# Performance work log

Measured on AMD Instinct MI355X. Metric: run time of the kernel, lower is better.

Reference implementation:

```python
import jax, jax.numpy as jnp
import numpy as np

G = 8          # n_games
D_IN = 512     # per-game input dim (equal for all games)
H1 = 1024
H2 = 1024
A = 128        # max_actions
B = 8192       # batch rows


def setup_inputs() -> dict:
    key = jax.random.key(0)
    ks = jax.random.split(key, 9)
    state = jax.random.normal(ks[0], (B, D_IN), dtype=jnp.float32)
    idx = jax.random.randint(ks[1], (B,), 0, G, dtype=jnp.int32)
    # per-game input linears: uniform(-1/sqrt(fan_in), 1/sqrt(fan_in))
    lim1 = 1.0 / np.sqrt(D_IN)
    W1 = jax.random.uniform(ks[2], (G, D_IN, H1), minval=-lim1, maxval=lim1, dtype=jnp.float32)
    b1 = jax.random.uniform(ks[3], (G, H1), minval=-lim1, maxval=lim1, dtype=jnp.float32)
    # shared linear
    lim2 = 1.0 / np.sqrt(H1)
    W2 = jax.random.uniform(ks[4], (H1, H2), minval=-lim2, maxval=lim2, dtype=jnp.float32)
    b2 = jax.random.uniform(ks[5], (H2,), minval=-lim2, maxval=lim2, dtype=jnp.float32)
    # per-game output heads: uniform(-0.003, 0.003)
    W3 = jax.random.uniform(ks[6], (G, H2, A), minval=-0.003, maxval=0.003, dtype=jnp.float32)
    b3 = jax.random.uniform(ks[7], (G, A), minval=-0.003, maxval=0.003, dtype=jnp.float32)
    return {"state": state, "idx": idx, "W1": W1, "b1": b1, "W2": W2, "b2": b2, "W3": W3, "b3": b3}


def reference(state, idx, W1, b1, W2, b2, W3, b3):
    # Torch code concatenates per-game groups in sorted-unique-idx order,
    # i.e. a stable permutation of rows by idx; reproduce exactly.
    perm = jnp.argsort(idx, stable=True)          # [B]
    s = state[perm]                               # [B, D_IN]
    g = idx[perm]                                 # [B] game of each permuted row
    # routed first layer: compute all games then gather per-row game
    h1_all = jnp.einsum('bd,gdh->bgh', s, W1) + b1            # [B, G, H1]
    h1 = jax.nn.relu(jnp.take_along_axis(h1_all, g[:, None, None], axis=1)[:, 0, :])  # [B, H1]
    h_f = jax.nn.relu(h1 @ W2 + b2)                            # [B, H2]
    a = jnp.tanh(jnp.einsum('bh,gha->bga', h_f, W3) + b3)      # [B, G, A]
    # NOTE: original gathers heads with the ORIGINAL (unpermuted) idx,
    # even though rows of `a` are in permuted order. Reproduce faithfully.
    out = jnp.take_along_axis(a, idx[:, None, None], axis=1)[:, 0, :]  # [B, A]
    return out
```

## Files before the change

kernel.cpp:

```cpp
#include <hip/hip_runtime.h>
#include <math.h>

#define G_GAMES 8
#define D_IN 512
#define H1 1024
#define H2 1024
#define A_DIM 128
#define B_ROWS 8192

typedef short bf16x8 __attribute__((ext_vector_type(8)));
typedef float f32x4 __attribute__((ext_vector_type(4)));

#define WS_OFF   0u
#define WS_PERM  256u
#define WS_SPERM 33280u
#define WS_W1T   (WS_SPERM + B_ROWS*D_IN*2u)
#define WS_W2T   (WS_W1T + G_GAMES*D_IN*H1*2u)
#define WS_W3T   (WS_W2T + (unsigned)H1*H2*2u)
#define WS_H1    (WS_W3T + G_GAMES*H2*A_DIM*2u)
#define WS_HF    WS_SPERM

__device__ __forceinline__ unsigned short f2bf(float x) {
  union { float f; unsigned int u; } v; v.f = x;
  unsigned int r = v.u + 0x7fffu + ((v.u >> 16) & 1u);
  return (unsigned short)(r >> 16);
}

__device__ __forceinline__ void async_load16(const void* gptr, void* ldsptr) {
  __builtin_amdgcn_global_load_lds(
      (const __attribute__((address_space(1))) unsigned int*)gptr,
      (__attribute__((address_space(3))) unsigned int*)ldsptr,
      16, 0, 0);
}

__device__ void sort_256(const int* __restrict__ idx, int* __restrict__ perm,
                         int* __restrict__ off) {
  __shared__ int wtot[4][9];
  __shared__ int wbase[4][9];
  __shared__ int offs[9];
  const int t = threadIdx.x, lane = t & 63, wave = t >> 6;
  int my[32];
#pragma unroll
  for (int i = 0; i < 8; ++i) {
    const int4 a = *(const int4*)(idx + t * 32 + i * 4);
    my[i*4+0] = a.x; my[i*4+1] = a.y; my[i*4+2] = a.z; my[i*4+3] = a.w;
  }
  int local[8] = {0,0,0,0,0,0,0,0};
#pragma unroll
  for (int i = 0; i < 32; ++i) local[my[i]]++;
  int incl[8];
#pragma unroll
  for (int g = 0; g < 8; ++g) {
    int v = local[g];
#pragma unroll
    for (int d = 1; d < 64; d <<= 1) {
      const int n = __shfl_up(v, d);
      if (lane >= d) v += n;
    }
    incl[g] = v;
  }
  if (lane == 63) {
#pragma unroll
    for (int g = 0; g < 8; ++g) wtot[wave][g] = incl[g];
  }
  __syncthreads();
  if (t < 8) {
    int s = 0;
#pragma unroll
    for (int w = 0; w < 4; ++w) { wbase[w][t] = s; s += wtot[w][t]; }
    wtot[0][t] = s;
  }
  __syncthreads();
  if (t == 0) {
    int s = 0;
#pragma unroll
    for (int g = 0; g < 8; ++g) { offs[g] = s; off[g] = s; s += wtot[0][g]; }
    offs[8] = s; off[8] = s;
  }
  __syncthreads();
  int start[8];
#pragma unroll
  for (int g = 0; g < 8; ++g)
    start[g] = offs[g] + wbase[wave][g] + (incl[g] - local[g]);
#pragma unroll
  for (int i = 0; i < 32; ++i) {
    const int g = my[i];
    perm[start[g]++] = t * 32 + i;
  }
}

__device__ void trans_tile(const float* __restrict__ in,
                           unsigned short* __restrict__ out,
                           int R, int C, int xt, int yt, int z) {
  in  += (size_t)z * R * C;
  out += (size_t)z * R * C;
  __shared__ float tile[64][65];
  const int c0 = xt * 64, r0 = yt * 64;
  const int tx = threadIdx.x & 63, ty = threadIdx.x >> 6;
#pragma unroll
  for (int rr = ty; rr < 64; rr += 4)
    tile[rr][tx] = in[(size_t)(r0 + rr) * C + c0 + tx];
  __syncthreads();
#pragma unroll
  for (int cc = ty; cc < 64; cc += 4)
    out[(size_t)(c0 + cc) * R + r0 + tx] = f2bf(tile[tx][cc]);
}

__global__ __launch_bounds__(256) void k_pre1(const float* __restrict__ W1,
                                              const float* __restrict__ W2,
                                              const float* __restrict__ W3,
                                              const int* __restrict__ idx,
                                              unsigned short* __restrict__ W1T,
                                              unsigned short* __restrict__ W2T,
                                              unsigned short* __restrict__ W3T,
                                              int* __restrict__ perm,
                                              int* __restrict__ off) {
  const int b = blockIdx.x;
  if (b < 1024) {
    const int z = b >> 7, r = b & 127;
    trans_tile(W1, W1T, D_IN, H1, r & 15, r >> 4, z);
  } else if (b < 1280) {
    const int r = b - 1024;
    trans_tile(W2, W2T, H1, H2, r & 15, r >> 4, 0);
  } else if (b < 1536) {
    const int r = (b - 1280) & 31, z = (b - 1280) >> 5;
    trans_tile(W3, W3T, H2, A_DIM, r & 1, r >> 1, z);
  } else {
    sort_256(idx, perm, off);
  }
}

__global__ __launch_bounds__(256) void k_gather(const float* __restrict__ state,
                                                const int* __restrict__ perm,
                                                unsigned short* __restrict__ sPerm) {
  const int p = blockIdx.x * 2 + (threadIdx.x >> 7);
  const int c = (threadIdx.x & 127) << 2;
  const int src = perm[p];
  const float4 v = *(const float4*)(state + (size_t)src * D_IN + c);
  ushort4 o;
  o.x = f2bf(v.x); o.y = f2bf(v.y); o.z = f2bf(v.z); o.w = f2bf(v.w);
  *(ushort4*)(sPerm + (size_t)p * D_IN + c) = o;
}

template <int KTOT>
__device__ __forceinline__ void gemm_db_core(const unsigned short* const* aP,
                                             const unsigned short* const* bP,
                                             char* smem, int tid, f32x4 acc[4][4]) {
  const int lane = tid & 63, wave = tid >> 6;
  const int wm = wave & 1, wn = wave >> 1;
  const int sw = lane & 15, quad = lane >> 4;
  const int mA = wm * 64 + sw;
  const int nB = wn * 64 + sw;
  char* A0 = smem;          char* A1 = smem + 16384;
  char* B0 = smem + 32768;  char* B1 = smem + 49152;
  const int NIT = KTOT >> 6;
#pragma unroll
  for (int c = 0; c < 4; ++c) {
    async_load16(aP[c], A0 + (wave * 32 + c * 8) * 128);
    async_load16(bP[c], B0 + (wave * 32 + c * 8) * 128);
  }
#pragma unroll 2
  for (int k = 0; k < NIT; ++k) {
    __syncthreads();
    char* A = (k & 1) ? A1 : A0;
    char* B = (k & 1) ? B1 : B0;
    if (k + 1 < NIT) {
      char* An = (k & 1) ? A0 : A1;
      char* Bn = (k & 1) ? B0 : B1;
      const int koff = (k + 1) << 6;
#pragma unroll
      for (int c = 0; c < 4; ++c) {
        async_load16(aP[c] + koff, An + (wave * 32 + c * 8) * 128);
        async_load16(bP[c] + koff, Bn + (wave * 32 + c * 8) * 128);
      }
    }
#pragma unroll
    for (int ks = 0; ks < 2; ++ks) {
      const int u = ((((ks << 2) + quad) ^ (sw & 7)) << 4);
      bf16x8 aF[4], bF[4];
#pragma unroll
      for (int i = 0; i < 4; ++i) {
        aF[i] = *(const bf16x8*)(A + (mA + i * 16) * 128 + u);
        bF[i] = *(const bf16x8*)(B + (nB + i * 16) * 128 + u);
      }
#pragma unroll
      for (int i = 0; i < 4; ++i)
#pragma unroll
        for (int j = 0; j < 4; ++j)
          acc[i][j] = __builtin_amdgcn_mfma_f32_16x16x32_bf16(aF[i], bF[j], acc[i][j], 0, 0, 0);
    }
  }
}

__device__ __forceinline__ bool seg_map(const int* __restrict__ off, int T,
                                        int& g, int& seg1, int& row0) {
  int base = 0;
  for (int gg = 0; gg < 8; ++gg) {
    const int s = off[gg], e = off[gg + 1];
    const int nt = (e - s + 127) >> 7;
    if (T < base + nt) { g = gg; seg1 = e; row0 = s + (T - base) * 128; return true; }
    base += nt;
  }
  return false;
}

__device__ __forceinline__ bool seg_map32(const int* __restrict__ off, int T,
                                          int& g, int& seg1, int& row0) {
  int base = 0;
  for (int gg = 0; gg < 8; ++gg) {
    const int s = off[gg], e = off[gg + 1];
    const int nt = (e - s + 31) >> 5;
    if (T < base + nt) { g = gg; seg1 = e; row0 = s + (T - base) * 32; return true; }
    base += nt;
  }
  return false;
}

__device__ __forceinline__ void epilogue_bf16(char* smem, const f32x4 acc[4][4],
                                              const float* bj, int tid,
                                              unsigned short* __restrict__ outp,
                                              size_t ldOut, int row0, int col0,
                                              int vrows) {
  const int lane = tid & 63, wave = tid >> 6;
  const int wm = wave & 1, wn = wave >> 1;
  const int sw = lane & 15, quad = lane >> 4;
  __syncthreads();
#pragma unroll
  for (int i = 0; i < 4; ++i)
#pragma unroll
    for (int j = 0; j < 4; ++j)
#pragma unroll
      for (int r = 0; r < 4; ++r) {
        const int row = wm * 64 + i * 16 + quad * 4 + r;
        const int col = wn * 64 + j * 16 + sw;
        const float v = fmaxf(acc[i][j][r] + bj[j], 0.0f);
        *(unsigned short*)(smem + row * 264 + col * 2) = f2bf(v);
      }
  __syncthreads();
#pragma unroll
  for (int q = 0; q < 8; ++q) {
    const int idxq = q * 256 + tid;
    const int row = idxq >> 4, ch = idxq & 15;
    if (row < vrows) {
      const uint2 lo = *(const uint2*)(smem + row * 264 + ch * 16);
      const uint2 hi = *(const uint2*)(smem + row * 264 + ch * 16 + 8);
      uint4 v; v.x = lo.x; v.y = lo.y; v.z = hi.x; v.w = hi.y;
      *(uint4*)((char*)outp + ((size_t)(row0 + row) * ldOut + col0 + ch * 8) * 2) = v;
    }
  }
}

__global__ __launch_bounds__(256) void k_gemm1(const unsigned short* __restrict__ sPerm,
                                               const unsigned short* __restrict__ W1T,
                                               const float* __restrict__ b1,
                                               const int* __restrict__ off,
                                               unsigned short* __restrict__ h1out) {
  __shared__ char smem[65536];
  int g, seg1, row0;
  if (!seg_map(off, blockIdx.x, g, seg1, row0)) return;
  const int col0 = blockIdx.y * 128;
  const int tid = threadIdx.x, lane = tid & 63, wave = tid >> 6;
  const int gcol = ((lane & 7) ^ (lane >> 3)) << 3;
  const unsigned short* aP[4];
  const unsigned short* bP[4];
#pragma unroll
  for (int c = 0; c < 4; ++c) {
    const int rl = wave * 32 + c * 8 + (lane >> 3);
    int p = row0 + rl;
    if (p > seg1 - 1) p = seg1 - 1;
    aP[c] = sPerm + (size_t)p * D_IN + gcol;
    bP[c] = W1T + (size_t)g * H1 * D_IN + (size_t)(col0 + rl) * D_IN + gcol;
  }
  f32x4 acc[4][4] = {};
  gemm_db_core<D_IN>(aP, bP, smem, tid, acc);
  const int wn = wave >> 1, sw = lane & 15;
  const float* bg = b1 + g * H1;
  float bj[4];
#pragma unroll
  for (int j = 0; j < 4; ++j) bj[j] = bg[col0 + wn * 64 + j * 16 + sw];
  const int vrows = min(128, seg1 - row0);
  epilogue_bf16(smem, acc, bj, tid, h1out, H1, row0, col0, vrows);
}

__global__ __launch_bounds__(256) void k_gemm2(const unsigned short* __restrict__ h1in,
                                               const unsigned short* __restrict__ W2T,
                                               const float* __restrict__ b2,
                                               unsigned short* __restrict__ hfout) {
  __shared__ char smem[65536];
  const int row0 = blockIdx.x * 128, col0 = blockIdx.y * 128;
  const int tid = threadIdx.x, lane = tid & 63, wave = tid >> 6;
  const int gcol = ((lane & 7) ^ (lane >> 3)) << 3;
  const unsigned short* aP[4];
  const unsigned short* bP[4];
#pragma unroll
  for (int c = 0; c < 4; ++c) {
    const int rl = wave * 32 + c * 8 + (lane >> 3);
    aP[c] = h1in + (size_t)(row0 + rl) * H1 + gcol;
    bP[c] = W2T + (size_t)(col0 + rl) * H1 + gcol;
  }
  f32x4 acc[4][4] = {};
  gemm_db_core<H1>(aP, bP, smem, tid, acc);
  const int wn = wave >> 1, sw = lane & 15;
  float bj[4];
#pragma unroll
  for (int j = 0; j < 4; ++j) bj[j] = b2[col0 + wn * 64 + j * 16 + sw];
  epilogue_bf16(smem, acc, bj, tid, hfout, H2, row0, col0, 128);
}

__global__ __launch_bounds__(256) void k_gemm3(const unsigned short* __restrict__ hf,
                                               const unsigned short* __restrict__ W3T,
                                               const float* __restrict__ b3,
                                               const int* __restrict__ off,
                                               const int* __restrict__ perm,
                                               float* __restrict__ outp) {
  __shared__ char smem[40960];
  int g, seg1, row0;
  if (!seg_map32(off, blockIdx.x, g, seg1, row0)) return;
  const int tid = threadIdx.x, lane = tid & 63, wave = tid >> 6;
  const int wm = wave & 1, wn = wave >> 1;
  const int sw = lane & 15, quad = lane >> 4;
  const int gcol = ((lane & 7) ^ (lane >> 3)) << 3;
  int q0 = row0 + wave * 8 + (lane >> 3);
  if (q0 > seg1 - 1) q0 = seg1 - 1;
  const unsigned short* aP = hf + (size_t)perm[q0] * H2 + gcol;
  const unsigned short* bP[4];
#pragma unroll
  for (int c = 0; c < 4; ++c) {
    const int rl = wave * 32 + c * 8 + (lane >> 3);
    bP[c] = W3T + (size_t)g * A_DIM * H2 + (size_t)rl * H2 + gcol;
  }
  char* A0 = smem;         char* A1 = smem + 4096;
  char* B0 = smem + 8192;  char* B1 = smem + 24576;
  const int mA = wm * 16 + sw;
  const int nB = wn * 64 + sw;
  f32x4 acc[4] = {};
  async_load16(aP, A0 + (wave * 8) * 128);
#pragma unroll
  for (int c = 0; c < 4; ++c)
    async_load16(bP[c], B0 + (wave * 32 + c * 8) * 128);
#pragma unroll 2
  for (int k = 0; k < (H2 >> 6); ++k) {
    __syncthreads();
    char* A = (k & 1) ? A1 : A0;
    char* B = (k & 1) ? B1 : B0;
    if (k + 1 < (H2 >> 6)) {
      char* An = (k & 1) ? A0 : A1;
      char* Bn = (k & 1) ? B0 : B1;
      const int koff = (k + 1) << 6;
      async_load16(aP + koff, An + (wave * 8) * 128);
#pragma unroll
      for (int c = 0; c < 4; ++c)
        async_load16(bP[c] + koff, Bn + (wave * 32 + c * 8) * 128);
    }
#pragma unroll
    for (int ks = 0; ks < 2; ++ks) {
      const int u = ((((ks << 2) + quad) ^ (sw & 7)) << 4);
      const bf16x8 aF = *(const bf16x8*)(A + mA * 128 + u);
      bf16x8 bF[4];
#pragma unroll
      for (int j = 0; j < 4; ++j)
        bF[j] = *(const bf16x8*)(B + (nB + j * 16) * 128 + u);
#pragma unroll
      for (int j = 0; j < 4; ++j)
        acc[j] = __builtin_amdgcn_mfma_f32_16x16x32_bf16(aF, bF[j], acc[j], 0, 0, 0);
    }
  }
  const float* bg = b3 + g * A_DIM;
  float bj[4];
#pragma unroll
  for (int j = 0; j < 4; ++j) bj[j] = bg[wn * 64 + j * 16 + sw];
  __syncthreads();
#pragma unroll
  for (int j = 0; j < 4; ++j)
#pragma unroll
    for (int r = 0; r < 4; ++r) {
      const int row = wm * 16 + quad * 4 + r;
      const int col = wn * 64 + j * 16 + sw;
      *(float*)(smem + row * 528 + col * 4) = tanhf(acc[j][r] + bj[j]);
    }
  __syncthreads();
#pragma unroll
  for (int qq = 0; qq < 4; ++qq) {
    const int idxq = qq * 256 + tid;
    const int row = idxq >> 5, ch = idxq & 31;
    if (row0 + row < seg1) {
      const uint4 v = *(const uint4*)(smem + row * 528 + ch * 16);
      *(uint4*)((char*)outp + ((size_t)perm[row0 + row] * A_DIM + ch * 4) * 4) = v;
    }
  }
}

extern "C" void kernel_launch(void* const* d_in, const int* in_sizes, int n_in,
                              void* d_out, int out_size, void* d_ws, size_t ws_size,
                              hipStream_t stream) {
  (void)in_sizes; (void)n_in; (void)out_size; (void)ws_size;
  const float* state = (const float*)d_in[0];
  const int*   idx   = (const int*)d_in[1];
  const float* W1    = (const float*)d_in[2];
  const float* b1    = (const float*)d_in[3];
  const float* W2    = (const float*)d_in[4];
  const float* b2    = (const float*)d_in[5];
  const float* W3    = (const float*)d_in[6];
  const float* b3    = (const float*)d_in[7];
  float* outp = (float*)d_out;
  char* ws = (char*)d_ws;
  int* off  = (int*)(ws + WS_OFF);
  int* perm = (int*)(ws + WS_PERM);
  unsigned short* sPerm = (unsigned short*)(ws + WS_SPERM);
  unsigned short* W1T   = (unsigned short*)(ws + WS_W1T);
  unsigned short* W2T   = (unsigned short*)(ws + WS_W2T);
  unsigned short* W3T   = (unsigned short*)(ws + WS_W3T);
  unsigned short* h1    = (unsigned short*)(ws + WS_H1);
  unsigned short* hf    = (unsigned short*)(ws + WS_HF);

  hipLaunchKernelGGL(k_pre1, dim3(1537), dim3(256), 0, stream,
                     W1, W2, W3, idx, W1T, W2T, W3T, perm, off);
  hipLaunchKernelGGL(k_gather, dim3(B_ROWS / 2), dim3(256), 0, stream, state, perm, sPerm);
  hipLaunchKernelGGL(k_gemm1, dim3(72, 8), dim3(256), 0, stream, sPerm, W1T, b1, off, h1);
  hipLaunchKernelGGL(k_gemm2, dim3(64, 8), dim3(256), 0, stream, h1, W2T, b2, hf);
  hipLaunchKernelGGL(k_gemm3, dim3(264), dim3(256), 0, stream, hf, W3T, b3, off, perm, outp);
}
```

Measured before the change: 155.6 us.

## Load weight B fragments directly from global memory instead of staging in LDS

All three GEMM kernels stop staging the weight (B) tiles through shared memory. Each wave now reads its bf16x8 MFMA fragments straight from global memory inside the k-loop, and only the activation (A) tiles stay double-buffered in LDS. This cuts LDS use per block (64KB to about 33KB), which may allow more blocks per CU, and removes the LDS write and read for B. The cost is that the global B loads are no longer prefetched, so their latency sits exposed right before the MFMAs. Each fragment read is also a strided 16-byte access, and the two waves sharing the same N columns now fetch them redundantly.

```diff
diff --git a/kernel.cpp b/kernel.cpp
--- a/kernel.cpp
+++ b/kernel.cpp
@@ -143,46 +143,41 @@
 }
 
 template <int KTOT>
-__device__ __forceinline__ void gemm_db_core(const unsigned short* const* aP,
-                                             const unsigned short* const* bP,
+__device__ __forceinline__ void gemm_bd_core(const unsigned short* const* aP,
+                                             const unsigned short* __restrict__ bBase,
                                              char* smem, int tid, f32x4 acc[4][4]) {
   const int lane = tid & 63, wave = tid >> 6;
-  const int wm = wave & 1, wn = wave >> 1;
+  const int wm = wave & 1;
   const int sw = lane & 15, quad = lane >> 4;
   const int mA = wm * 64 + sw;
-  const int nB = wn * 64 + sw;
-  char* A0 = smem;          char* A1 = smem + 16384;
-  char* B0 = smem + 32768;  char* B1 = smem + 49152;
+  char* A0 = smem;
+  char* A1 = smem + 16384;
   const int NIT = KTOT >> 6;
 #pragma unroll
-  for (int c = 0; c < 4; ++c) {
+  for (int c = 0; c < 4; ++c)
     async_load16(aP[c], A0 + (wave * 32 + c * 8) * 128);
-    async_load16(bP[c], B0 + (wave * 32 + c * 8) * 128);
-  }
 #pragma unroll 2
   for (int k = 0; k < NIT; ++k) {
     __syncthreads();
     char* A = (k & 1) ? A1 : A0;
-    char* B = (k & 1) ? B1 : B0;
     if (k + 1 < NIT) {
       char* An = (k & 1) ? A0 : A1;
-      char* Bn = (k & 1) ? B0 : B1;
       const int koff = (k + 1) << 6;
 #pragma unroll
-      for (int c = 0; c < 4; ++c) {
+      for (int c = 0; c < 4; ++c)
         async_load16(aP[c] + koff, An + (wave * 32 + c * 8) * 128);
-        async_load16(bP[c] + koff, Bn + (wave * 32 + c * 8) * 128);
-      }
     }
 #pragma unroll
     for (int ks = 0; ks < 2; ++ks) {
       const int u = ((((ks << 2) + quad) ^ (sw & 7)) << 4);
+      const int kg = (k << 6) + (ks << 5);
       bf16x8 aF[4], bF[4];
 #pragma unroll
-      for (int i = 0; i < 4; ++i) {
+      for (int j = 0; j < 4; ++j)
+        bF[j] = *(const bf16x8*)(bBase + (size_t)j * 16 * KTOT + kg);
+#pragma unroll
+      for (int i = 0; i < 4; ++i)
         aF[i] = *(const bf16x8*)(A + (mA + i * 16) * 128 + u);
-        bF[i] = *(const bf16x8*)(B + (nB + i * 16) * 128 + u);
-      }
 #pragma unroll
       for (int i = 0; i < 4; ++i)
 #pragma unroll
@@ -255,25 +250,26 @@
                                                const float* __restrict__ b1,
                                                const int* __restrict__ off,
                                                unsigned short* __restrict__ h1out) {
-  __shared__ char smem[65536];
+  __shared__ char smem[33792];
   int g, seg1, row0;
   if (!seg_map(off, blockIdx.x, g, seg1, row0)) return;
   const int col0 = blockIdx.y * 128;
   const int tid = threadIdx.x, lane = tid & 63, wave = tid >> 6;
+  const int sw = lane & 15, quad = lane >> 4;
   const int gcol = ((lane & 7) ^ (lane >> 3)) << 3;
   const unsigned short* aP[4];
-  const unsigned short* bP[4];
 #pragma unroll
   for (int c = 0; c < 4; ++c) {
     const int rl = wave * 32 + c * 8 + (lane >> 3);
     int p = row0 + rl;
     if (p > seg1 - 1) p = seg1 - 1;
     aP[c] = sPerm + (size_t)p * D_IN + gcol;
-    bP[c] = W1T + (size_t)g * H1 * D_IN + (size_t)(col0 + rl) * D_IN + gcol;
-  }
+  }
+  const unsigned short* bBase =
+      W1T + (size_t)g * H1 * D_IN + (size_t)(col0 + (wave >> 1) * 64 + sw) * D_IN + quad * 8;
   f32x4 acc[4][4] = {};
-  gemm_db_core<D_IN>(aP, bP, smem, tid, acc);
-  const int wn = wave >> 1, sw = lane & 15;
+  gemm_bd_core<D_IN>(aP, bBase, smem, tid, acc);
+  const int wn = wave >> 1;
   const float* bg = b1 + g * H1;
   float bj[4];
 #pragma unroll
@@ -286,21 +282,22 @@
                                                const unsigned short* __restrict__ W2T,
                                                const float* __restrict__ b2,
                                                unsigned short* __restrict__ hfout) {
-  __shared__ char smem[65536];
+  __shared__ char smem[33792];
   const int row0 = blockIdx.x * 128, col0 = blockIdx.y * 128;
   const int tid = threadIdx.x, lane = tid & 63, wave = tid >> 6;
+  const int sw = lane & 15, quad = lane >> 4;
   const int gcol = ((lane & 7) ^ (lane >> 3)) << 3;
   const unsigned short* aP[4];
-  const unsigned short* bP[4];
 #pragma unroll
   for (int c = 0; c < 4; ++c) {
     const int rl = wave * 32 + c * 8 + (lane >> 3);
     aP[c] = h1in + (size_t)(row0 + rl) * H1 + gcol;
-    bP[c] = W2T + (size_t)(col0 + rl) * H1 + gcol;
-  }
+  }
+  const unsigned short* bBase =
+      W2T + (size_t)(col0 + (wave >> 1) * 64 + sw) * H1 + quad * 8;
   f32x4 acc[4][4] = {};
-  gemm_db_core<H1>(aP, bP, smem, tid, acc);
-  const int wn = wave >> 1, sw = lane & 15;
+  gemm_bd_core<H1>(aP, bBase, smem, tid, acc);
+  const int wn = wave >> 1;
   float bj[4];
 #pragma unroll
   for (int j = 0; j < 4; ++j) bj[j] = b2[col0 + wn * 64 + j * 16 + sw];
@@ -313,7 +310,7 @@
                                                const int* __restrict__ off,
                                                const int* __restrict__ perm,
                                                float* __restrict__ outp) {
-  __shared__ char smem[40960];
+  __shared__ char smem[16896];
   int g, seg1, row0;
   if (!seg_map32(off, blockIdx.x, g, seg1, row0)) return;
   const int tid = threadIdx.x, lane = tid & 63, wave = tid >> 6;
@@ -323,43 +320,30 @@
   int q0 = row0 + wave * 8 + (lane >> 3);
   if (q0 > seg1 - 1) q0 = seg1 - 1;
   const unsigned short* aP = hf + (size_t)perm[q0] * H2 + gcol;
-  const unsigned short* bP[4];
-#pragma unroll
-  for (int c = 0; c < 4; ++c) {
-    const int rl = wave * 32 + c * 8 + (lane >> 3);
-    bP[c] = W3T + (size_t)g * A_DIM * H2 + (size_t)rl * H2 + gcol;
-  }
-  char* A0 = smem;         char* A1 = smem + 4096;
-  char* B0 = smem + 8192;  char* B1 = smem + 24576;
+  const unsigned short* bBase =
+      W3T + (size_t)g * A_DIM * H2 + (size_t)(wn * 64 + sw) * H2 + quad * 8;
+  char* A0 = smem;
+  char* A1 = smem + 4096;
   const int mA = wm * 16 + sw;
-  const int nB = wn * 64 + sw;
   f32x4 acc[4] = {};
   async_load16(aP, A0 + (wave * 8) * 128);
-#pragma unroll
-  for (int c = 0; c < 4; ++c)
-    async_load16(bP[c], B0 + (wave * 32 + c * 8) * 128);
 #pragma unroll 2
   for (int k = 0; k < (H2 >> 6); ++k) {
     __syncthreads();
     char* A = (k & 1) ? A1 : A0;
-    char* B = (k & 1) ? B1 : B0;
     if (k + 1 < (H2 >> 6)) {
       char* An = (k & 1) ? A0 : A1;
-      char* Bn = (k & 1) ? B0 : B1;
-      const int koff = (k + 1) << 6;
-      async_load16(aP + koff, An + (wave * 8) * 128);
-#pragma unroll
-      for (int c = 0; c < 4; ++c)
-        async_load16(bP[c] + koff, Bn + (wave * 32 + c * 8) * 128);
+      async_load16(aP + ((k + 1) << 6), An + (wave * 8) * 128);
     }
 #pragma unroll
     for (int ks = 0; ks < 2; ++ks) {
       const int u = ((((ks << 2) + quad) ^ (sw & 7)) << 4);
+      const int kg = (k << 6) + (ks << 5);
       const bf16x8 aF = *(const bf16x8*)(A + mA * 128 + u);
       bf16x8 bF[4];
 #pragma unroll
       for (int j = 0; j < 4; ++j)
-        bF[j] = *(const bf16x8*)(B + (nB + j * 16) * 128 + u);
+        bF[j] = *(const bf16x8*)(bBase + (size_t)j * 16 * H2 + kg);
 #pragma unroll
       for (int j = 0; j < 4; ++j)
         acc[j] = __builtin_amdgcn_mfma_f32_16x16x32_bf16(aF, bF[j], acc[j], 0, 0, 0);
```

New measurement: 209.4 us. 1.35x slower.

## Fuse row gather and bf16 conversion into gemm1 A-tile loads; XCD-aware gemm2 grid

Applied to the files above, without the earlier changes.

Removes the separate gather kernel. gemm1 now reads permuted fp32 state rows directly through perm, converts them to bf16 in registers and writes them into swizzled LDS while the previous tile computes. This drops one launch and the sPerm round trip through global memory. In exchange, A loads now go through registers as synchronous global loads, and each 128-row tile is re-read by all 8 column blocks. gemm2 also switches to a 1D grid remapped so blocks on the same XCD share the same row tiles, aiming for better L2 reuse.

```diff
diff --git a/kernel.cpp b/kernel.cpp
--- a/kernel.cpp
+++ b/kernel.cpp
@@ -130,16 +130,157 @@
   }
 }
 
-__global__ __launch_bounds__(256) void k_gather(const float* __restrict__ state,
-                                                const int* __restrict__ perm,
-                                                unsigned short* __restrict__ sPerm) {
-  const int p = blockIdx.x * 2 + (threadIdx.x >> 7);
-  const int c = (threadIdx.x & 127) << 2;
-  const int src = perm[p];
-  const float4 v = *(const float4*)(state + (size_t)src * D_IN + c);
-  ushort4 o;
-  o.x = f2bf(v.x); o.y = f2bf(v.y); o.z = f2bf(v.z); o.w = f2bf(v.w);
-  *(ushort4*)(sPerm + (size_t)p * D_IN + c) = o;
+__device__ __forceinline__ bool seg_map(const int* __restrict__ off, int T,
+                                        int& g, int& seg1, int& row0) {
+  int base = 0;
+  for (int gg = 0; gg < 8; ++gg) {
+    const int s = off[gg], e = off[gg + 1];
+    const int nt = (e - s + 127) >> 7;
+    if (T < base + nt) { g = gg; seg1 = e; row0 = s + (T - base) * 128; return true; }
+    base += nt;
+  }
+  return false;
+}
+
+__device__ __forceinline__ bool seg_map32(const int* __restrict__ off, int T,
+                                          int& g, int& seg1, int& row0) {
+  int base = 0;
+  for (int gg = 0; gg < 8; ++gg) {
+    const int s = off[gg], e = off[gg + 1];
+    const int nt = (e - s + 31) >> 5;
+    if (T < base + nt) { g = gg; seg1 = e; row0 = s + (T - base) * 32; return true; }
+    base += nt;
+  }
+  return false;
+}
+
+__device__ __forceinline__ void epilogue_bf16(char* smem, const f32x4 acc[4][4],
+                                              const float* bj, int tid,
+                                              unsigned short* __restrict__ outp,
+                                              size_t ldOut, int row0, int col0,
+                                              int vrows) {
+  const int lane = tid & 63, wave = tid >> 6;
+  const int wm = wave & 1, wn = wave >> 1;
+  const int sw = lane & 15, quad = lane >> 4;
+  __syncthreads();
+#pragma unroll
+  for (int i = 0; i < 4; ++i)
+#pragma unroll
+    for (int j = 0; j < 4; ++j)
+#pragma unroll
+      for (int r = 0; r < 4; ++r) {
+        const int row = wm * 64 + i * 16 + quad * 4 + r;
+        const int col = wn * 64 + j * 16 + sw;
+        const float v = fmaxf(acc[i][j][r] + bj[j], 0.0f);
+        *(unsigned short*)(smem + row * 264 + col * 2) = f2bf(v);
+      }
+  __syncthreads();
+#pragma unroll
+  for (int q = 0; q < 8; ++q) {
+    const int idxq = q * 256 + tid;
+    const int row = idxq >> 4, ch = idxq & 15;
+    if (row < vrows) {
+      const uint2 lo = *(const uint2*)(smem + row * 264 + ch * 16);
+      const uint2 hi = *(const uint2*)(smem + row * 264 + ch * 16 + 8);
+      uint4 v; v.x = lo.x; v.y = lo.y; v.z = hi.x; v.w = hi.y;
+      *(uint4*)((char*)outp + ((size_t)(row0 + row) * ldOut + col0 + ch * 8) * 2) = v;
+    }
+  }
+}
+
+__device__ __forceinline__ void write_a_row(char* Ab, const float4* pv, int r, int h) {
+#pragma unroll
+  for (int j = 0; j < 4; ++j) {
+    const float4 a = pv[2 * j], b = pv[2 * j + 1];
+    uint4 w;
+    w.x = (unsigned)f2bf(a.x) | ((unsigned)f2bf(a.y) << 16);
+    w.y = (unsigned)f2bf(a.z) | ((unsigned)f2bf(a.w) << 16);
+    w.z = (unsigned)f2bf(b.x) | ((unsigned)f2bf(b.y) << 16);
+    w.w = (unsigned)f2bf(b.z) | ((unsigned)f2bf(b.w) << 16);
+    *(uint4*)(Ab + r * 128 + (((h * 4 + j) ^ (r & 7)) << 4)) = w;
+  }
+}
+
+__global__ __launch_bounds__(256) void k_gemm1(const float* __restrict__ state,
+                                               const int* __restrict__ perm,
+                                               const unsigned short* __restrict__ W1T,
+                                               const float* __restrict__ b1,
+                                               const int* __restrict__ off,
+                                               unsigned short* __restrict__ h1out) {
+  __shared__ char smem[65536];
+  int g, seg1, row0;
+  if (!seg_map(off, blockIdx.x, g, seg1, row0)) return;
+  const int col0 = blockIdx.y * 128;
+  const int tid = threadIdx.x, lane = tid & 63, wave = tid >> 6;
+  const int gcol = ((lane & 7) ^ (lane >> 3)) << 3;
+  const int r = tid >> 1, h = tid & 1;
+  int p = row0 + r;
+  if (p > seg1 - 1) p = seg1 - 1;
+  const float4* aSrc4 = (const float4*)(state + (size_t)perm[p] * D_IN) + h * 8;
+  const unsigned short* bP[4];
+#pragma unroll
+  for (int c = 0; c < 4; ++c) {
+    const int rl = wave * 32 + c * 8 + (lane >> 3);
+    bP[c] = W1T + (size_t)g * H1 * D_IN + (size_t)(col0 + rl) * D_IN + gcol;
+  }
+  char* A0 = smem;          char* A1 = smem + 16384;
+  char* B0 = smem + 32768;  char* B1 = smem + 49152;
+  const int sw = lane & 15, quad = lane >> 4;
+  const int wm = wave & 1;
+  const int mA = wm * 64 + sw;
+  const int nB = (wave >> 1) * 64 + sw;
+  f32x4 acc[4][4] = {};
+  {
+    float4 pv[8];
+#pragma unroll
+    for (int q = 0; q < 8; ++q) pv[q] = aSrc4[q];
+#pragma unroll
+    for (int c = 0; c < 4; ++c)
+      async_load16(bP[c], B0 + (wave * 32 + c * 8) * 128);
+    write_a_row(A0, pv, r, h);
+  }
+  const int NIT = D_IN >> 6;
+#pragma unroll 2
+  for (int k = 0; k < NIT; ++k) {
+    __syncthreads();
+    char* A = (k & 1) ? A1 : A0;
+    char* B = (k & 1) ? B1 : B0;
+    float4 pv[8];
+    const bool pre = (k + 1 < NIT);
+    if (pre) {
+      const int fo = (k + 1) * 16;
+#pragma unroll
+      for (int q = 0; q < 8; ++q) pv[q] = aSrc4[fo + q];
+      char* Bn = (k & 1) ? B0 : B1;
+      const int koff = (k + 1) << 6;
+#pragma unroll
+      for (int c = 0; c < 4; ++c)
+        async_load16(bP[c] + koff, Bn + (wave * 32 + c * 8) * 128);
+    }
+#pragma unroll
+    for (int ks = 0; ks < 2; ++ks) {
+      const int u = ((((ks << 2) + quad) ^ (sw & 7)) << 4);
+      bf16x8 aF[4], bF[4];
+#pragma unroll
+      for (int i = 0; i < 4; ++i) {
+        aF[i] = *(const bf16x8*)(A + (mA + i * 16) * 128 + u);
+        bF[i] = *(const bf16x8*)(B + (nB + i * 16) * 128 + u);
+      }
+#pragma unroll
+      for (int i = 0; i < 4; ++i)
+#pragma unroll
+        for (int j = 0; j < 4; ++j)
+          acc[i][j] = __builtin_amdgcn_mfma_f32_16x16x32_bf16(aF[i], bF[j], acc[i][j], 0, 0, 0);
+    }
+    if (pre) write_a_row((k & 1) ? A0 : A1, pv, r, h);
+  }
+  const int wn = wave >> 1;
+  const float* bg = b1 + g * H1;
+  float bj[4];
+#pragma unroll
+  for (int j = 0; j < 4; ++j) bj[j] = bg[col0 + wn * 64 + j * 16 + sw];
+  const int vrows = min(128, seg1 - row0);
+  epilogue_bf16(smem, acc, bj, tid, h1out, H1, row0, col0, vrows);
 }
 
 template <int KTOT>
@@ -192,102 +333,15 @@
   }
 }
 
-__device__ __forceinline__ bool seg_map(const int* __restrict__ off, int T,
-                                        int& g, int& seg1, int& row0) {
-  int base = 0;
-  for (int gg = 0; gg < 8; ++gg) {
-    const int s = off[gg], e = off[gg + 1];
-    const int nt = (e - s + 127) >> 7;
-    if (T < base + nt) { g = gg; seg1 = e; row0 = s + (T - base) * 128; return true; }
-    base += nt;
-  }
-  return false;
-}
-
-__device__ __forceinline__ bool seg_map32(const int* __restrict__ off, int T,
-                                          int& g, int& seg1, int& row0) {
-  int base = 0;
-  for (int gg = 0; gg < 8; ++gg) {
-    const int s = off[gg], e = off[gg + 1];
-    const int nt = (e - s + 31) >> 5;
-    if (T < base + nt) { g = gg; seg1 = e; row0 = s + (T - base) * 32; return true; }
-    base += nt;
-  }
-  return false;
-}
-
-__device__ __forceinline__ void epilogue_bf16(char* smem, const f32x4 acc[4][4],
-                                              const float* bj, int tid,
-                                              unsigned short* __restrict__ outp,
-                                              size_t ldOut, int row0, int col0,
-                                              int vrows) {
-  const int lane = tid & 63, wave = tid >> 6;
-  const int wm = wave & 1, wn = wave >> 1;
-  const int sw = lane & 15, quad = lane >> 4;
-  __syncthreads();
-#pragma unroll
-  for (int i = 0; i < 4; ++i)
-#pragma unroll
-    for (int j = 0; j < 4; ++j)
-#pragma unroll
-      for (int r = 0; r < 4; ++r) {
-        const int row = wm * 64 + i * 16 + quad * 4 + r;
-        const int col = wn * 64 + j * 16 + sw;
-        const float v = fmaxf(acc[i][j][r] + bj[j], 0.0f);
-        *(unsigned short*)(smem + row * 264 + col * 2) = f2bf(v);
-      }
-  __syncthreads();
-#pragma unroll
-  for (int q = 0; q < 8; ++q) {
-    const int idxq = q * 256 + tid;
-    const int row = idxq >> 4, ch = idxq & 15;
-    if (row < vrows) {
-      const uint2 lo = *(const uint2*)(smem + row * 264 + ch * 16);
-      const uint2 hi = *(const uint2*)(smem + row * 264 + ch * 16 + 8);
-      uint4 v; v.x = lo.x; v.y = lo.y; v.z = hi.x; v.w = hi.y;
-      *(uint4*)((char*)outp + ((size_t)(row0 + row) * ldOut + col0 + ch * 8) * 2) = v;
-    }
-  }
-}
-
-__global__ __launch_bounds__(256) void k_gemm1(const unsigned short* __restrict__ sPerm,
-                                               const unsigned short* __restrict__ W1T,
-                                               const float* __restrict__ b1,
-                                               const int* __restrict__ off,
-                                               unsigned short* __restrict__ h1out) {
-  __shared__ char smem[65536];
-  int g, seg1, row0;
-  if (!seg_map(off, blockIdx.x, g, seg1, row0)) return;
-  const int col0 = blockIdx.y * 128;
-  const int tid = threadIdx.x, lane = tid & 63, wave = tid >> 6;
-  const int gcol = ((lane & 7) ^ (lane >> 3)) << 3;
-  const unsigned short* aP[4];
-  const unsigned short* bP[4];
-#pragma unroll
-  for (int c = 0; c < 4; ++c) {
-    const int rl = wave * 32 + c * 8 + (lane >> 3);
-    int p = row0 + rl;
-    if (p > seg1 - 1) p = seg1 - 1;
-    aP[c] = sPerm + (size_t)p * D_IN + gcol;
-    bP[c] = W1T + (size_t)g * H1 * D_IN + (size_t)(col0 + rl) * D_IN + gcol;
-  }
-  f32x4 acc[4][4] = {};
-  gemm_db_core<D_IN>(aP, bP, smem, tid, acc);
-  const int wn = wave >> 1, sw = lane & 15;
-  const float* bg = b1 + g * H1;
-  float bj[4];
-#pragma unroll
-  for (int j = 0; j < 4; ++j) bj[j] = bg[col0 + wn * 64 + j * 16 + sw];
-  const int vrows = min(128, seg1 - row0);
-  epilogue_bf16(smem, acc, bj, tid, h1out, H1, row0, col0, vrows);
-}
-
 __global__ __launch_bounds__(256) void k_gemm2(const unsigned short* __restrict__ h1in,
                                                const unsigned short* __restrict__ W2T,
                                                const float* __restrict__ b2,
                                                unsigned short* __restrict__ hfout) {
   __shared__ char smem[65536];
-  const int row0 = blockIdx.x * 128, col0 = blockIdx.y * 128;
+  const int bid = blockIdx.x;
+  const int xcd = bid & 7, slot = bid >> 3;
+  const int row0 = (xcd * 8 + (slot & 7)) * 128;
+  const int col0 = (slot >> 3) * 128;
   const int tid = threadIdx.x, lane = tid & 63, wave = tid >> 6;
   const int gcol = ((lane & 7) ^ (lane >> 3)) << 3;
   const unsigned short* aP[4];
@@ -406,7 +460,6 @@
   char* ws = (char*)d_ws;
   int* off  = (int*)(ws + WS_OFF);
   int* perm = (int*)(ws + WS_PERM);
-  unsigned short* sPerm = (unsigned short*)(ws + WS_SPERM);
   unsigned short* W1T   = (unsigned short*)(ws + WS_W1T);
   unsigned short* W2T   = (unsigned short*)(ws + WS_W2T);
   unsigned short* W3T   = (unsigned short*)(ws + WS_W3T);
@@ -415,8 +468,8 @@
 
   hipLaunchKernelGGL(k_pre1, dim3(1537), dim3(256), 0, stream,
                      W1, W2, W3, idx, W1T, W2T, W3T, perm, off);
-  hipLaunchKernelGGL(k_gather, dim3(B_ROWS / 2), dim3(256), 0, stream, state, perm, sPerm);
-  hipLaunchKernelGGL(k_gemm1, dim3(72, 8), dim3(256), 0, stream, sPerm, W1T, b1, off, h1);
-  hipLaunchKernelGGL(k_gemm2, dim3(64, 8), dim3(256), 0, stream, h1, W2T, b2, hf);
+  hipLaunchKernelGGL(k_gemm1, dim3(72, 8), dim3(256), 0, stream,
+                     state, perm, W1T, b1, off, h1);
+  hipLaunchKernelGGL(k_gemm2, dim3(512), dim3(256), 0, stream, h1, W2T, b2, hf);
   hipLaunchKernelGGL(k_gemm3, dim3(264), dim3(256), 0, stream, hf, W3T, b3, off, perm, outp);
 }
```

After: 167.5 us. +7.6%, slower.
